# Kernel tuning notes

Hardware: AMD Instinct MI355X
Metric: run time of the kernel (lower is better)

The kernel has to match this reference:

```python
import jax, jax.numpy as jnp
import numpy as np

ROWS, N = 2048, 32768  # kernel requires N = 8 tiles * 1024 threads * 4 (float4)

def setup_inputs() -> dict:
    key = jax.random.key(0)
    kx, km = jax.random.split(key)
    x = jax.random.normal(kx, (ROWS, N), dtype=jnp.float32)
    mask = jax.random.randint(km, (ROWS, N), 0, 2).astype(jnp.bool_)
    return {"x": x, "mask": mask}

def reference(x, mask):
    # Masked inclusive cumulative sum along dim=1: cumsum(where(mask, x, 0))
    return jnp.cumsum(jnp.where(mask, x, jnp.float32(0)), axis=1)
```

## Files before the change

### kernel.cpp

```cpp
#include <hip/hip_runtime.h>


#define ROWS    2048
#define NCOL    32768
#define THREADS 1024
#define TILES   8
#define NCHUNK  (THREADS * TILES)

__global__ __launch_bounds__(THREADS, 1) void masked_cumsum_kernel(
    const float* __restrict__ x,
    const int*   __restrict__ mask,
    float*       __restrict__ out)
{
    const int row = blockIdx.x;
    const size_t base = (size_t)row * NCOL;
    const float4* __restrict__ xrow = (const float4*)(x + base);
    const int4*   __restrict__ mrow = (const int4*)(mask + base);
    float4*       __restrict__ orow = (float4*)(out + base);

    const int tid  = threadIdx.x;
    const int lane = tid & 63;
    const int wave = tid >> 6;

    __shared__ float csum[NCHUNK + NCHUNK / 8];
    __shared__ float wtot[16];

    float4 xv[TILES];
    int4   mv[TILES];
    #pragma unroll
    for (int t = 0; t < TILES; ++t) {
        xv[t] = xrow[t * THREADS + tid];
        mv[t] = mrow[t * THREADS + tid];
    }

    float4 p[TILES];
    #pragma unroll
    for (int t = 0; t < TILES; ++t) {
        float a0 = mv[t].x ? xv[t].x : 0.0f;
        float a1 = mv[t].y ? xv[t].y : 0.0f;
        float a2 = mv[t].z ? xv[t].z : 0.0f;
        float a3 = mv[t].w ? xv[t].w : 0.0f;
        p[t].x = a0;
        p[t].y = p[t].x + a1;
        p[t].z = p[t].y + a2;
        p[t].w = p[t].z + a3;
        int c = t * THREADS + tid;
        csum[c + (c >> 3)] = p[t].w;
    }
    __syncthreads();

    float s[8];
    float run = 0.0f;
    #pragma unroll
    for (int k = 0; k < 8; ++k) {
        run += csum[tid * 9 + k];
        s[k] = run;
    }

    float sc = run;
    #pragma unroll
    for (int d = 1; d < 64; d <<= 1) {
        float o = __shfl_up(sc, d);
        if (lane >= d) sc += o;
    }
    if (lane == 63) wtot[wave] = sc;
    __syncthreads();

    float woff = 0.0f;
    #pragma unroll
    for (int w = 0; w < 16; ++w)
        woff += (w < wave) ? wtot[w] : 0.0f;

    const float thr_excl = woff + (sc - run);

    #pragma unroll
    for (int k = 0; k < 8; ++k)
        csum[tid * 9 + k] = thr_excl + (k ? s[k - 1] : 0.0f);
    __syncthreads();

    #pragma unroll
    for (int t = 0; t < TILES; ++t) {
        int c = t * THREADS + tid;
        float off = csum[c + (c >> 3)];
        orow[t * THREADS + tid] =
            make_float4(off + p[t].x, off + p[t].y, off + p[t].z, off + p[t].w);
    }
}

extern "C" void kernel_launch(void* const* d_in, const int* in_sizes, int n_in,
                              void* d_out, int out_size, void* d_ws, size_t ws_size,
                              hipStream_t stream) {
    const float* x    = (const float*)d_in[0];
    const int*   mask = (const int*)d_in[1];
    float*       out  = (float*)d_out;
    masked_cumsum_kernel<<<ROWS, THREADS, 0, stream>>>(x, mask, out);
}
```

Baseline: 570.2 us.

## Split rows into segments with chained decoupled-lookback prefix across blocks

Each row is split into 8 segments of 4096 columns, each handled by a 256-thread block, so far more blocks run at once with smaller per-block register and shared-memory footprints. Segments pass their running row prefix through flags in the workspace: each block spins on its predecessor's flag, then publishes its own inclusive total. Blocks are ordered segment-major so predecessors are dispatched first, which avoids deadlock. This adds a memset of the flag buffer plus a serial chain of global atomic waits along each row, and keeps the old per-row kernel as a fallback when no workspace is provided.

```diff
diff --git a/kernel.cpp b/kernel.cpp
--- a/kernel.cpp
+++ b/kernel.cpp
@@ -3,57 +3,64 @@
 
 #define ROWS    2048
 #define NCOL    32768
-#define THREADS 1024
-#define TILES   8
-#define NCHUNK  (THREADS * TILES)
+#define SEGCOL  4096
+#define NSEG    (NCOL / SEGCOL)
+#define THREADS 256
+#define CPT     4
+#define NCH     (THREADS * CPT)
+#define PAD(i)  ((i) + ((i) >> 2))
 
-__global__ __launch_bounds__(THREADS, 1) void masked_cumsum_kernel(
+__global__ __launch_bounds__(THREADS, 8) void mcs_chain(
     const float* __restrict__ x,
     const int*   __restrict__ mask,
-    float*       __restrict__ out)
+    float*       __restrict__ out,
+    unsigned long long* __restrict__ done)
 {
-    const int row = blockIdx.x;
-    const size_t base = (size_t)row * NCOL;
-    const float4* __restrict__ xrow = (const float4*)(x + base);
-    const int4*   __restrict__ mrow = (const int4*)(mask + base);
-    float4*       __restrict__ orow = (float4*)(out + base);
+    const int bid = blockIdx.x;
+    const int seg = bid >> 11;
+    const int row = bid & 2047;
+    const size_t base = (size_t)row * NCOL + (size_t)seg * SEGCOL;
+    const float4* __restrict__ xs = (const float4*)(x + base);
+    const int4*   __restrict__ ms = (const int4*)(mask + base);
+    float4*       __restrict__ os = (float4*)(out + base);
 
     const int tid  = threadIdx.x;
     const int lane = tid & 63;
     const int wave = tid >> 6;
 
-    __shared__ float csum[NCHUNK + NCHUNK / 8];
-    __shared__ float wtot[16];
+    __shared__ float csum[PAD(NCH - 1) + 2];
+    __shared__ float wtot[4];
+    __shared__ float bcast;
 
-    float4 xv[TILES];
-    int4   mv[TILES];
+    float4 xv[CPT];
+    int4   mv[CPT];
     #pragma unroll
-    for (int t = 0; t < TILES; ++t) {
-        xv[t] = xrow[t * THREADS + tid];
-        mv[t] = mrow[t * THREADS + tid];
+    for (int k = 0; k < CPT; ++k) {
+        xv[k] = xs[k * THREADS + tid];
+        mv[k] = ms[k * THREADS + tid];
     }
 
-    float4 p[TILES];
+    float4 p[CPT];
     #pragma unroll
-    for (int t = 0; t < TILES; ++t) {
-        float a0 = mv[t].x ? xv[t].x : 0.0f;
-        float a1 = mv[t].y ? xv[t].y : 0.0f;
-        float a2 = mv[t].z ? xv[t].z : 0.0f;
-        float a3 = mv[t].w ? xv[t].w : 0.0f;
-        p[t].x = a0;
-        p[t].y = p[t].x + a1;
-        p[t].z = p[t].y + a2;
-        p[t].w = p[t].z + a3;
-        int c = t * THREADS + tid;
-        csum[c + (c >> 3)] = p[t].w;
+    for (int k = 0; k < CPT; ++k) {
+        float a0 = mv[k].x ? xv[k].x : 0.0f;
+        float a1 = mv[k].y ? xv[k].y : 0.0f;
+        float a2 = mv[k].z ? xv[k].z : 0.0f;
+        float a3 = mv[k].w ? xv[k].w : 0.0f;
+        p[k].x = a0;
+        p[k].y = p[k].x + a1;
+        p[k].z = p[k].y + a2;
+        p[k].w = p[k].z + a3;
+        int c = k * THREADS + tid;
+        csum[PAD(c)] = p[k].w;
     }
     __syncthreads();
 
-    float s[8];
+    float s[CPT];
     float run = 0.0f;
     #pragma unroll
-    for (int k = 0; k < 8; ++k) {
-        run += csum[tid * 9 + k];
+    for (int k = 0; k < CPT; ++k) {
+        run += csum[PAD(tid * CPT + k)];
         s[k] = run;
     }
 
@@ -68,22 +75,98 @@
 
     float woff = 0.0f;
     #pragma unroll
-    for (int w = 0; w < 16; ++w)
+    for (int w = 0; w < 4; ++w)
         woff += (w < wave) ? wtot[w] : 0.0f;
-
     const float thr_excl = woff + (sc - run);
 
     #pragma unroll
-    for (int k = 0; k < 8; ++k)
-        csum[tid * 9 + k] = thr_excl + (k ? s[k - 1] : 0.0f);
+    for (int k = 0; k < CPT; ++k)
+        csum[PAD(tid * CPT + k)] = thr_excl + (k ? s[k - 1] : 0.0f);
+
+    if (tid == 0) {
+        float btot = wtot[0] + wtot[1] + wtot[2] + wtot[3];
+        float excl = 0.0f;
+        if (seg != 0) {
+            const unsigned long long* pred = done + (bid - ROWS);
+            unsigned long long v;
+            do {
+                v = __hip_atomic_load(pred, __ATOMIC_ACQUIRE,
+                                      __HIP_MEMORY_SCOPE_AGENT);
+                if ((v >> 32) == 1ull) break;
+                __builtin_amdgcn_s_sleep(1);
+            } while (true);
+            excl = __uint_as_float((unsigned)v);
+        }
+        unsigned long long pv =
+            (1ull << 32) | (unsigned long long)__float_as_uint(excl + btot);
+        __hip_atomic_store(done + bid, pv, __ATOMIC_RELEASE,
+                           __HIP_MEMORY_SCOPE_AGENT);
+        bcast = excl;
+    }
     __syncthreads();
 
+    const float ro = bcast;
     #pragma unroll
-    for (int t = 0; t < TILES; ++t) {
-        int c = t * THREADS + tid;
+    for (int k = 0; k < CPT; ++k) {
+        int c = k * THREADS + tid;
+        float off = ro + csum[PAD(c)];
+        os[c] = make_float4(off + p[k].x, off + p[k].y, off + p[k].z,
+                            off + p[k].w);
+    }
+}
+
+#define FB_THREADS 1024
+#define FB_TILES   8
+#define FB_NCHUNK  (FB_THREADS * FB_TILES)
+
+__global__ __launch_bounds__(FB_THREADS, 1) void mcs_fallback(
+    const float* __restrict__ x, const int* __restrict__ mask,
+    float* __restrict__ out)
+{
+    const int row = blockIdx.x;
+    const size_t base = (size_t)row * NCOL;
+    const float4* xrow = (const float4*)(x + base);
+    const int4*   mrow = (const int4*)(mask + base);
+    float4*       orow = (float4*)(out + base);
+    const int tid = threadIdx.x, lane = tid & 63, wave = tid >> 6;
+    __shared__ float csum[FB_NCHUNK + FB_NCHUNK / 8];
+    __shared__ float wt[16];
+    float4 xv[FB_TILES]; int4 mv[FB_TILES];
+    #pragma unroll
+    for (int t = 0; t < FB_TILES; ++t) {
+        xv[t] = xrow[t * FB_THREADS + tid];
+        mv[t] = mrow[t * FB_THREADS + tid];
+    }
+    float4 p[FB_TILES];
+    #pragma unroll
+    for (int t = 0; t < FB_TILES; ++t) {
+        float a0 = mv[t].x ? xv[t].x : 0.f, a1 = mv[t].y ? xv[t].y : 0.f;
+        float a2 = mv[t].z ? xv[t].z : 0.f, a3 = mv[t].w ? xv[t].w : 0.f;
+        p[t].x = a0; p[t].y = p[t].x + a1; p[t].z = p[t].y + a2; p[t].w = p[t].z + a3;
+        int c = t * FB_THREADS + tid;
+        csum[c + (c >> 3)] = p[t].w;
+    }
+    __syncthreads();
+    float s[8], run = 0.f;
+    #pragma unroll
+    for (int k = 0; k < 8; ++k) { run += csum[tid * 9 + k]; s[k] = run; }
+    float sc = run;
+    #pragma unroll
+    for (int d = 1; d < 64; d <<= 1) { float o = __shfl_up(sc, d); if (lane >= d) sc += o; }
+    if (lane == 63) wt[wave] = sc;
+    __syncthreads();
+    float woff = 0.f;
+    #pragma unroll
+    for (int w = 0; w < 16; ++w) woff += (w < wave) ? wt[w] : 0.f;
+    const float te = woff + (sc - run);
+    #pragma unroll
+    for (int k = 0; k < 8; ++k) csum[tid * 9 + k] = te + (k ? s[k - 1] : 0.f);
+    __syncthreads();
+    #pragma unroll
+    for (int t = 0; t < FB_TILES; ++t) {
+        int c = t * FB_THREADS + tid;
         float off = csum[c + (c >> 3)];
-        orow[t * THREADS + tid] =
-            make_float4(off + p[t].x, off + p[t].y, off + p[t].z, off + p[t].w);
+        orow[c] = make_float4(off + p[t].x, off + p[t].y, off + p[t].z, off + p[t].w);
     }
 }
 
@@ -93,5 +176,13 @@
     const float* x    = (const float*)d_in[0];
     const int*   mask = (const int*)d_in[1];
     float*       out  = (float*)d_out;
-    masked_cumsum_kernel<<<ROWS, THREADS, 0, stream>>>(x, mask, out);
+    const size_t flag_bytes = (size_t)NSEG * ROWS * sizeof(unsigned long long);
+
+    if (d_ws != nullptr && ws_size >= flag_bytes) {
+        hipMemsetAsync(d_ws, 0, flag_bytes, stream);
+        mcs_chain<<<NSEG * ROWS, THREADS, 0, stream>>>(
+            x, mask, out, (unsigned long long*)d_ws);
+    } else {
+        mcs_fallback<<<ROWS, FB_THREADS, 0, stream>>>(x, mask, out);
+    }
 }
```

Result: slower. 1.393 ms (+144.3%).
